# Kernel optimization log

Measured on AMD Instinct MI355X. Metric: run time of the kernel, lower is better.

Reference implementation:

```python
import jax, jax.numpy as jnp
import numpy as np

B, T, D = 4, 1024, 1024   # batch, block_size, d_model
H, HS = 16, 64            # n_head, head_size


def setup_inputs() -> dict:
    key = jax.random.key(0)
    ks = jax.random.split(key, 6)
    s = 0.02  # small init like nn.Linear default scale
    return {
        "x": jax.random.normal(ks[0], (B, T, D), jnp.float32),
        "Wq": jax.random.normal(ks[1], (H, D, HS), jnp.float32) * s,
        "Wk": jax.random.normal(ks[2], (H, D, HS), jnp.float32) * s,
        "Wv": jax.random.normal(ks[3], (H, D, HS), jnp.float32) * s,
        "Wo": jax.random.normal(ks[4], (H * HS, D), jnp.float32) * s,
        "bo": jnp.zeros((D,), jnp.float32),
    }


def reference(x, Wq, Wk, Wv, Wo, bo):
    # Batched equivalent of the per-head loop: all heads in one einsum.
    q = jnp.einsum('btd,hde->bhte', x, Wq)   # [B,H,T,HS]
    k = jnp.einsum('btd,hde->bhte', x, Wk)
    v = jnp.einsum('btd,hde->bhte', x, Wv)
    scores = jnp.einsum('bhte,bhse->bhts', q, k) * (HS ** -0.5)  # [B,H,T,T]
    causal = jnp.tril(jnp.ones((T, T), dtype=bool))
    scores = jnp.where(causal, scores, -jnp.inf)
    att = jax.nn.softmax(scores, axis=-1)
    out = jnp.einsum('bhts,bhse->bhte', att, v)                  # [B,H,T,HS]
    out = out.transpose(0, 2, 1, 3).reshape(B, T, H * HS)        # concat heads
    return out @ Wo + bo                                         # proj to d_model
```

## Files before the change

kernel.cpp:

```cpp
#include <hip/hip_runtime.h>
#include <math.h>

#define NB 4
#define SEQ 1024
#define DM 1024
#define NH 16
#define HS 64

typedef __attribute__((ext_vector_type(8))) short short8;
typedef __attribute__((ext_vector_type(4))) short short4v;
typedef __attribute__((ext_vector_type(4))) float floatx4;

#define MFMA(a, b, c) __builtin_amdgcn_mfma_f32_16x16x32_bf16((a), (b), (c), 0, 0, 0)

static __device__ __forceinline__ unsigned short f2bf(float f) {
  unsigned int u = __float_as_uint(f);
  u += 0x7FFFu + ((u >> 16) & 1u);
  return (unsigned short)(u >> 16);
}
static __device__ __forceinline__ unsigned short f2bf_fast(float f) {
  return (unsigned short)((__float_as_uint(f) + 0x8000u) >> 16);
}

static __device__ __forceinline__ void g2l(const unsigned short* g, short* l) {
  __builtin_amdgcn_global_load_lds(
      (const __attribute__((address_space(1))) void*)g,
      (__attribute__((address_space(3))) void*)l, 16, 0, 0);
}

#define SWZ_SRC(tid) ((((tid) & 7) ^ (((tid) >> 3) & 7)) << 3)
#define SWZ_RD(B, r) ((((B) ^ ((r) & 7)) << 3))

__global__ __launch_bounds__(256) void prep_all(
    const float* __restrict__ x,
    const float* __restrict__ Wq, const float* __restrict__ Wk,
    const float* __restrict__ Wv, const float* __restrict__ Wo,
    unsigned short* __restrict__ xb,
    unsigned short* __restrict__ Wtq, unsigned short* __restrict__ Wtk,
    unsigned short* __restrict__ Wtv, unsigned short* __restrict__ Wot) {
  __shared__ __align__(16) short Ts[64 * 72];
  const int tid = threadIdx.x;
  const int mat = blockIdx.y;
  if (mat == 4) {
    int base = blockIdx.x * 4096;
#pragma unroll
    for (int i = 0; i < 16; i++) {
      int idx4 = base + tid + i * 256;
      float4 v = *(const float4*)(x + (size_t)idx4 * 4);
      short4v o;
      o[0] = (short)f2bf(v.x); o[1] = (short)f2bf(v.y);
      o[2] = (short)f2bf(v.z); o[3] = (short)f2bf(v.w);
      *(short4v*)(xb + (size_t)idx4 * 4) = o;
    }
    return;
  }
  const float* src;
  unsigned short* dst;
  int r0, c0;
  if (mat < 3) {
    src = (mat == 0) ? Wq : (mat == 1) ? Wk : Wv;
    dst = (mat == 0) ? Wtq : (mat == 1) ? Wtk : Wtv;
    int h = blockIdx.x >> 4;
    int d0 = (blockIdx.x & 15) * 64;
    src += (size_t)(h * DM + d0) * HS;
    dst += (size_t)(h * HS) * DM + d0;
    r0 = HS;  c0 = DM;
  } else {
    src = Wo; dst = Wot;
    int k0 = (blockIdx.x >> 4) * 64;
    int n0 = (blockIdx.x & 15) * 64;
    src += (size_t)k0 * DM + n0;
    dst += (size_t)n0 * DM + k0;
    r0 = DM;  c0 = DM;
  }
#pragma unroll
  for (int i = 0; i < 4; i++) {
    int p = tid + i * 256;
    int row = p >> 4, c4 = (p & 15) << 2;
    float4 v = *(const float4*)(src + (size_t)row * r0 + c4);
    Ts[(c4 + 0) * 72 + row] = (short)f2bf(v.x);
    Ts[(c4 + 1) * 72 + row] = (short)f2bf(v.y);
    Ts[(c4 + 2) * 72 + row] = (short)f2bf(v.z);
    Ts[(c4 + 3) * 72 + row] = (short)f2bf(v.w);
  }
  __syncthreads();
#pragma unroll
  for (int i = 0; i < 2; i++) {
    int p = tid + i * 256;
    int row = p >> 3, c8 = (p & 7) << 3;
    *(short8*)(dst + (size_t)row * c0 + c8) = *(const short8*)&Ts[row * 72 + c8];
  }
}

__global__ __launch_bounds__(256, 3) void qkv_gemm128(
    const unsigned short* __restrict__ xb,
    const unsigned short* __restrict__ Wcat,
    unsigned short* __restrict__ qo,
    unsigned short* __restrict__ ko,
    unsigned short* __restrict__ vo) {
  __shared__ __align__(16) short As[128 * 64];
  __shared__ __align__(16) short Bs[128 * 64];
  const int tid = threadIdx.x;
  const int bm = blockIdx.x, bn = blockIdx.y;
  const int lane = tid & 63, wave = tid >> 6;
  const int quad = lane >> 4, l16 = lane & 15;
  const int wr = wave >> 1, wc = wave & 1;
  const int l7 = l16 & 7;
  const floatx4 fzero = {0.f, 0.f, 0.f, 0.f};

  floatx4 acc[4][4];
#pragma unroll
  for (int i = 0; i < 4; i++)
#pragma unroll
    for (int j = 0; j < 4; j++) acc[i][j] = fzero;

  const int srow = tid >> 3;
  const int scolw = SWZ_SRC(tid);
  const unsigned short* Ag = xb + (size_t)(bm * 128 + srow) * DM + scolw;
  const unsigned short* Bg = Wcat + (size_t)(bn * 128 + srow) * DM + scolw;
  short* Ad = As + tid * 8;
  short* Bd = Bs + tid * 8;

  for (int k0 = 0; k0 < DM; k0 += 64) {
    __syncthreads();
#pragma unroll
    for (int i = 0; i < 4; i++) g2l(Ag + (size_t)i * 32 * DM + k0, Ad + i * 2048);
#pragma unroll
    for (int i = 0; i < 4; i++) g2l(Bg + (size_t)i * 32 * DM + k0, Bd + i * 2048);
    __syncthreads();

    short8 af[4][2], bf[4][2];
#pragma unroll
    for (int ti = 0; ti < 4; ti++)
#pragma unroll
      for (int kh = 0; kh < 2; kh++)
        af[ti][kh] = *(const short8*)&As[(wr * 64 + ti * 16 + l16) * 64 +
                                          SWZ_RD(kh * 4 + quad, l7)];
#pragma unroll
    for (int tj = 0; tj < 4; tj++)
#pragma unroll
      for (int kh = 0; kh < 2; kh++)
        bf[tj][kh] = *(const short8*)&Bs[(wc * 64 + tj * 16 + l16) * 64 +
                                          SWZ_RD(kh * 4 + quad, l7)];
#pragma unroll
    for (int ti = 0; ti < 4; ti++)
#pragma unroll
      for (int tj = 0; tj < 4; tj++) {
        acc[ti][tj] = MFMA(af[ti][0], bf[tj][0], acc[ti][tj]);
        acc[ti][tj] = MFMA(af[ti][1], bf[tj][1], acc[ti][tj]);
      }
  }

  const int mat = bn >> 3;
  const int mbase = bm * 128 + wr * 64 + quad * 4;
  const int nn0 = (bn & 7) * 128 + wc * 64;
  if (mat < 2) {
    unsigned short* dst = (mat == 0) ? qo : ko;
#pragma unroll
    for (int ti = 0; ti < 4; ti++)
#pragma unroll
      for (int tj = 0; tj < 4; tj++) {
        int ecol = nn0 + tj * 16 + l16;
        int h = ecol >> 6, e = ecol & 63;
#pragma unroll
        for (int r = 0; r < 4; r++) {
          int m = mbase + ti * 16 + r;
          int b = m >> 10, t = m & (SEQ - 1);
          dst[((size_t)(b * NH + h) * SEQ + t) * HS + e] = f2bf_fast(acc[ti][tj][r]);
        }
      }
  } else {
#pragma unroll
    for (int ti = 0; ti < 4; ti++)
#pragma unroll
      for (int tj = 0; tj < 4; tj++) {
        int ecol = nn0 + tj * 16 + l16;
        int h = ecol >> 6, e = ecol & 63;
        int m0 = mbase + ti * 16;
        int b = m0 >> 10, t0 = m0 & (SEQ - 1);
        short4v pv;
#pragma unroll
        for (int r = 0; r < 4; r++) pv[r] = (short)f2bf_fast(acc[ti][tj][r]);
        *(short4v*)&vo[((size_t)(b * NH + h) * HS + e) * SEQ + t0] = pv;
      }
  }
}

__global__ __launch_bounds__(256) void attn_kernel(
    const unsigned short* __restrict__ q,
    const unsigned short* __restrict__ k,
    const unsigned short* __restrict__ v,
    unsigned short* __restrict__ o)
{
  __shared__ __align__(16) short Ks[64 * 64];
  __shared__ __align__(16) short Vt[64 * 64];
  __shared__ __align__(16) short Ps[64 * 76];
  const int tid = threadIdx.x;
  const int lid = (int)blockIdx.x;
  const int g = lid >> 8, cc = lid & 255;
  const int j = cc >> 6, bhid = cc & 63;
  const int qt = (g == 0) ? j : (g == 1) ? 15 - j : (g == 2) ? 7 - j : 8 + j;
  const int h = bhid & 15, b = bhid >> 4;
  const int lane = tid & 63, wave = tid >> 6;
  const int quad = lane >> 4, l16 = lane & 15;
  const int l7 = l16 & 7;
  const size_t bh = (size_t)(b * NH + h) * SEQ * HS;
  const unsigned short* qp = q + bh + (size_t)qt * 64 * HS;
  const unsigned short* kbase = k + bh;
  const unsigned short* vbase = v + (size_t)(b * NH + h) * HS * SEQ;
  const floatx4 fzero = {0.f, 0.f, 0.f, 0.f};
  const float c2 = 0.125f * 1.44269504089f;
  const float C0 = 16.0f * 1.44269504089f;
  const int srow = tid >> 3;
  const int scolw = SWZ_SRC(tid);

  short8 qa[2];
  qa[0] = *(const short8*)(qp + (size_t)(wave * 16 + l16) * HS + quad * 8);
  qa[1] = *(const short8*)(qp + (size_t)(wave * 16 + l16) * HS + 32 + quad * 8);

#pragma unroll
  for (int i = 0; i < 2; i++) {
    g2l(kbase + (size_t)(srow + i * 32) * HS + scolw, Ks + tid * 8 + i * 2048);
    g2l(vbase + (size_t)(srow + i * 32) * SEQ + scolw, Vt + tid * 8 + i * 2048);
  }
  __syncthreads();

  const int rowbase = qt * 64 + wave * 16;
  float l_[4];
  floatx4 O[4];
#pragma unroll
  for (int r = 0; r < 4; r++) l_[r] = 0.f;
#pragma unroll
  for (int tj = 0; tj < 4; tj++) O[tj] = fzero;

  for (int kt = 0; kt <= qt; kt++) {
    floatx4 S[4];
#pragma unroll
    for (int tj = 0; tj < 4; tj++) {
      short8 b0 = *(const short8*)&Ks[(tj * 16 + l16) * 64 + SWZ_RD(quad, l7)];
      short8 b1 = *(const short8*)&Ks[(tj * 16 + l16) * 64 + SWZ_RD(4 + quad, l7)];
      floatx4 s = fzero;
      s = MFMA(qa[0], b0, s);
      s = MFMA(qa[1], b1, s);
      S[tj] = s;
    }
    if (kt == qt) {
#pragma unroll
      for (int tj = 0; tj < 4; tj++) {
        int col = kt * 64 + tj * 16 + l16;
#pragma unroll
        for (int r = 0; r < 4; r++) {
          int row = rowbase + quad * 4 + r;
          if (col > row) S[tj][r] = -INFINITY;
        }
      }
    }
#pragma unroll
    for (int tj = 0; tj < 4; tj++)
#pragma unroll
      for (int r = 0; r < 4; r++) {
        float pv = __builtin_amdgcn_exp2f(S[tj][r] * c2 - C0);
        l_[r] += pv;
        Ps[(wave * 16 + quad * 4 + r) * 76 + tj * 16 + l16] =
            (short)(unsigned short)((__float_as_uint(pv) + 0x8000u) >> 16);
      }

    short8 pa[2];
#pragma unroll
    for (int kh = 0; kh < 2; kh++)
      pa[kh] = *(const short8*)&Ps[(wave * 16 + l16) * 76 + kh * 32 + quad * 8];
#pragma unroll
    for (int tj = 0; tj < 4; tj++) {
      short8 b0 = *(const short8*)&Vt[(tj * 16 + l16) * 64 + SWZ_RD(quad, l7)];
      short8 b1 = *(const short8*)&Vt[(tj * 16 + l16) * 64 + SWZ_RD(4 + quad, l7)];
      O[tj] = MFMA(pa[0], b0, O[tj]);
      O[tj] = MFMA(pa[1], b1, O[tj]);
    }

    if (kt < qt) {
      __syncthreads();
#pragma unroll
      for (int i = 0; i < 2; i++) {
        g2l(kbase + (size_t)(kt + 1) * 64 * HS + (size_t)(srow + i * 32) * HS + scolw,
            Ks + tid * 8 + i * 2048);
        g2l(vbase + (size_t)(srow + i * 32) * SEQ + (kt + 1) * 64 + scolw,
            Vt + tid * 8 + i * 2048);
      }
      __syncthreads();
    }
  }

#pragma unroll
  for (int r = 0; r < 4; r++) {
    float lsum = l_[r];
#pragma unroll
    for (int off = 1; off < 16; off <<= 1)
      lsum += __shfl_xor(lsum, off, 16);
    float inv = 1.0f / lsum;
#pragma unroll
    for (int tj = 0; tj < 4; tj++)
      Ps[(wave * 16 + quad * 4 + r) * 76 + tj * 16 + l16] =
          (short)f2bf_fast(O[tj][r] * inv);
  }
  __syncthreads();
  {
    const int row = tid >> 2;
    const int c16 = (tid & 3) * 16;
    unsigned short* dst = o + ((size_t)(b * SEQ + qt * 64 + row)) * DM + h * HS + c16;
    const short* src = &Ps[row * 76 + c16];
#pragma unroll
    for (int u = 0; u < 4; u++)
      *(short4v*)(dst + u * 4) = *(const short4v*)(src + u * 4);
  }
}

__global__ __launch_bounds__(256, 3) void out_gemm64(
    const unsigned short* __restrict__ A,
    const unsigned short* __restrict__ Bt,
    const float* __restrict__ bo,
    float* __restrict__ out) {
  __shared__ __align__(16) short As[128 * 64];
  __shared__ __align__(16) short Bs[64 * 64];
  const int tid = threadIdx.x;
  const int bm = blockIdx.x, bn = blockIdx.y;
  const int lane = tid & 63, wave = tid >> 6;
  const int quad = lane >> 4, l16 = lane & 15;
  const int wr = wave >> 1, wc = wave & 1;
  const int l7 = l16 & 7;
  const floatx4 fzero = {0.f, 0.f, 0.f, 0.f};

  floatx4 acc[4][2];
#pragma unroll
  for (int i = 0; i < 4; i++)
#pragma unroll
    for (int j = 0; j < 2; j++) acc[i][j] = fzero;

  const int srow = tid >> 3;
  const int scolw = SWZ_SRC(tid);
  const unsigned short* Ag = A + (size_t)(bm * 128 + srow) * DM + scolw;
  const unsigned short* Bg = Bt + (size_t)(bn * 64 + srow) * DM + scolw;
  short* Ad = As + tid * 8;
  short* Bd = Bs + tid * 8;

  for (int k0 = 0; k0 < DM; k0 += 64) {
    __syncthreads();
#pragma unroll
    for (int i = 0; i < 4; i++) g2l(Ag + (size_t)i * 32 * DM + k0, Ad + i * 2048);
#pragma unroll
    for (int i = 0; i < 2; i++) g2l(Bg + (size_t)i * 32 * DM + k0, Bd + i * 2048);
    __syncthreads();

    short8 af[4][2], bf[2][2];
#pragma unroll
    for (int ti = 0; ti < 4; ti++)
#pragma unroll
      for (int kh = 0; kh < 2; kh++)
        af[ti][kh] = *(const short8*)&As[(wr * 64 + ti * 16 + l16) * 64 +
                                          SWZ_RD(kh * 4 + quad, l7)];
#pragma unroll
    for (int tj = 0; tj < 2; tj++)
#pragma unroll
      for (int kh = 0; kh < 2; kh++)
        bf[tj][kh] = *(const short8*)&Bs[(wc * 32 + tj * 16 + l16) * 64 +
                                          SWZ_RD(kh * 4 + quad, l7)];
#pragma unroll
    for (int ti = 0; ti < 4; ti++)
#pragma unroll
      for (int tj = 0; tj < 2; tj++) {
        acc[ti][tj] = MFMA(af[ti][0], bf[tj][0], acc[ti][tj]);
        acc[ti][tj] = MFMA(af[ti][1], bf[tj][1], acc[ti][tj]);
      }
  }

#pragma unroll
  for (int ti = 0; ti < 4; ti++)
#pragma unroll
    for (int tj = 0; tj < 2; tj++) {
      int n = bn * 64 + wc * 32 + tj * 16 + l16;
      float bias = bo[n];
#pragma unroll
      for (int r = 0; r < 4; r++) {
        int m = bm * 128 + wr * 64 + ti * 16 + quad * 4 + r;
        out[(size_t)m * DM + n] = acc[ti][tj][r] + bias;
      }
    }
}

extern "C" void kernel_launch(void* const* d_in, const int* in_sizes, int n_in,
                              void* d_out, int out_size, void* d_ws, size_t ws_size,
                              hipStream_t stream) {
  const float* x  = (const float*)d_in[0];
  const float* Wq = (const float*)d_in[1];
  const float* Wk = (const float*)d_in[2];
  const float* Wv = (const float*)d_in[3];
  const float* Wo = (const float*)d_in[4];
  const float* bo = (const float*)d_in[5];
  float* out = (float*)d_out;

  const size_t nx = (size_t)NB * SEQ * DM;
  const size_t nw = (size_t)DM * DM;
  unsigned short* xb  = (unsigned short*)d_ws;
  unsigned short* wtq = xb + nx;
  unsigned short* wtk = wtq + nw;
  unsigned short* wtv = wtk + nw;
  unsigned short* wot = wtv + nw;
  unsigned short* qws = wot + nw;
  unsigned short* kws = qws + nx;
  unsigned short* vws = kws + nx;
  unsigned short* aws = vws + nx;

  prep_all<<<dim3(256, 5), dim3(256), 0, stream>>>(x, Wq, Wk, Wv, Wo,
                                                   xb, wtq, wtk, wtv, wot);
  qkv_gemm128<<<dim3(32, 24), dim3(256), 0, stream>>>(xb, wtq, qws, kws, vws);
  attn_kernel<<<dim3(1024), dim3(256), 0, stream>>>(qws, kws, vws, aws);
  out_gemm64<<<dim3(32, 16), dim3(256), 0, stream>>>(aws, wot, bo, out);
}
```

Measured before the change: 151.9 us.

## Load K/V fragments directly from global into registers, two waves of 32 rows

The attention kernel no longer stages K and V tiles in shared memory. Each lane now loads its MFMA fragments straight from global memory (relying on cache), which removes the two block-wide barriers per key tile. The block shrinks to two waves, each covering 32 query rows, so every loaded K/V fragment is reused across two 16-row sub-tiles. In exchange the kernel issues redundant global loads per wave, has no prefetch of the next tile, and needs more registers for the doubled accumulators.

```diff
diff --git a/kernel.cpp b/kernel.cpp
--- a/kernel.cpp
+++ b/kernel.cpp
@@ -186,14 +186,12 @@
   }
 }
 
-__global__ __launch_bounds__(256) void attn_kernel(
+__global__ __launch_bounds__(128) void attn_kernel(
     const unsigned short* __restrict__ q,
     const unsigned short* __restrict__ k,
     const unsigned short* __restrict__ v,
     unsigned short* __restrict__ o)
 {
-  __shared__ __align__(16) short Ks[64 * 64];
-  __shared__ __align__(16) short Vt[64 * 64];
   __shared__ __align__(16) short Ps[64 * 76];
   const int tid = threadIdx.x;
   const int lid = (int)blockIdx.x;
@@ -203,7 +201,6 @@
   const int h = bhid & 15, b = bhid >> 4;
   const int lane = tid & 63, wave = tid >> 6;
   const int quad = lane >> 4, l16 = lane & 15;
-  const int l7 = l16 & 7;
   const size_t bh = (size_t)(b * NH + h) * SEQ * HS;
   const unsigned short* qp = q + bh + (size_t)qt * 64 * HS;
   const unsigned short* kbase = k + bh;
@@ -211,105 +208,99 @@
   const floatx4 fzero = {0.f, 0.f, 0.f, 0.f};
   const float c2 = 0.125f * 1.44269504089f;
   const float C0 = 16.0f * 1.44269504089f;
-  const int srow = tid >> 3;
-  const int scolw = SWZ_SRC(tid);
-
-  short8 qa[2];
-  qa[0] = *(const short8*)(qp + (size_t)(wave * 16 + l16) * HS + quad * 8);
-  qa[1] = *(const short8*)(qp + (size_t)(wave * 16 + l16) * HS + 32 + quad * 8);
-
-#pragma unroll
-  for (int i = 0; i < 2; i++) {
-    g2l(kbase + (size_t)(srow + i * 32) * HS + scolw, Ks + tid * 8 + i * 2048);
-    g2l(vbase + (size_t)(srow + i * 32) * SEQ + scolw, Vt + tid * 8 + i * 2048);
-  }
-  __syncthreads();
-
-  const int rowbase = qt * 64 + wave * 16;
-  float l_[4];
-  floatx4 O[4];
-#pragma unroll
-  for (int r = 0; r < 4; r++) l_[r] = 0.f;
-#pragma unroll
-  for (int tj = 0; tj < 4; tj++) O[tj] = fzero;
+
+  short8 qa[2][2];
+#pragma unroll
+  for (int ih = 0; ih < 2; ih++)
+#pragma unroll
+    for (int kh = 0; kh < 2; kh++)
+      qa[ih][kh] = *(const short8*)(qp + (size_t)(wave * 32 + ih * 16 + l16) * HS +
+                                    kh * 32 + quad * 8);
+
+  const int rowbase = qt * 64 + wave * 32;
+  float l_[2][4];
+  floatx4 O[2][4];
+#pragma unroll
+  for (int ih = 0; ih < 2; ih++)
+#pragma unroll
+    for (int r = 0; r < 4; r++) l_[ih][r] = 0.f;
+#pragma unroll
+  for (int ih = 0; ih < 2; ih++)
+#pragma unroll
+    for (int tj = 0; tj < 4; tj++) O[ih][tj] = fzero;
 
   for (int kt = 0; kt <= qt; kt++) {
-    floatx4 S[4];
-#pragma unroll
-    for (int tj = 0; tj < 4; tj++) {
-      short8 b0 = *(const short8*)&Ks[(tj * 16 + l16) * 64 + SWZ_RD(quad, l7)];
-      short8 b1 = *(const short8*)&Ks[(tj * 16 + l16) * 64 + SWZ_RD(4 + quad, l7)];
-      floatx4 s = fzero;
-      s = MFMA(qa[0], b0, s);
-      s = MFMA(qa[1], b1, s);
-      S[tj] = s;
+    const unsigned short* kp = kbase + (size_t)kt * 64 * HS;
+    const unsigned short* vp = vbase + kt * 64;
+    short8 kb[4][2], vb[4][2];
+#pragma unroll
+    for (int tj = 0; tj < 4; tj++)
+#pragma unroll
+      for (int kh = 0; kh < 2; kh++) {
+        kb[tj][kh] = *(const short8*)(kp + (size_t)(tj * 16 + l16) * HS +
+                                      kh * 32 + quad * 8);
+        vb[tj][kh] = *(const short8*)(vp + (size_t)(tj * 16 + l16) * SEQ +
+                                      kh * 32 + quad * 8);
+      }
+    const bool diag = (kt == qt);
+#pragma unroll
+    for (int ih = 0; ih < 2; ih++)
+#pragma unroll
+      for (int tj = 0; tj < 4; tj++) {
+        floatx4 s = MFMA(qa[ih][0], kb[tj][0], fzero);
+        s = MFMA(qa[ih][1], kb[tj][1], s);
+        if (diag) {
+          int col = tj * 16 + l16;
+#pragma unroll
+          for (int r = 0; r < 4; r++)
+            if (col > wave * 32 + ih * 16 + quad * 4 + r) s[r] = -INFINITY;
+        }
+#pragma unroll
+        for (int r = 0; r < 4; r++) {
+          float pv = __builtin_amdgcn_exp2f(s[r] * c2 - C0);
+          l_[ih][r] += pv;
+          Ps[(wave * 32 + ih * 16 + quad * 4 + r) * 76 + tj * 16 + l16] =
+              (short)(unsigned short)((__float_as_uint(pv) + 0x8000u) >> 16);
+        }
+      }
+    short8 pa[2][2];
+#pragma unroll
+    for (int ih = 0; ih < 2; ih++)
+#pragma unroll
+      for (int kh = 0; kh < 2; kh++)
+        pa[ih][kh] = *(const short8*)&Ps[(wave * 32 + ih * 16 + l16) * 76 +
+                                          kh * 32 + quad * 8];
+#pragma unroll
+    for (int tj = 0; tj < 4; tj++)
+#pragma unroll
+      for (int ih = 0; ih < 2; ih++) {
+        O[ih][tj] = MFMA(pa[ih][0], vb[tj][0], O[ih][tj]);
+        O[ih][tj] = MFMA(pa[ih][1], vb[tj][1], O[ih][tj]);
+      }
+  }
+
+#pragma unroll
+  for (int ih = 0; ih < 2; ih++)
+#pragma unroll
+    for (int r = 0; r < 4; r++) {
+      float lsum = l_[ih][r];
+#pragma unroll
+      for (int off = 1; off < 16; off <<= 1)
+        lsum += __shfl_xor(lsum, off, 16);
+      float inv = 1.0f / lsum;
+#pragma unroll
+      for (int tj = 0; tj < 4; tj++)
+        Ps[(wave * 32 + ih * 16 + quad * 4 + r) * 76 + tj * 16 + l16] =
+            (short)f2bf_fast(O[ih][tj][r] * inv);
     }
-    if (kt == qt) {
-#pragma unroll
-      for (int tj = 0; tj < 4; tj++) {
-        int col = kt * 64 + tj * 16 + l16;
-#pragma unroll
-        for (int r = 0; r < 4; r++) {
-          int row = rowbase + quad * 4 + r;
-          if (col > row) S[tj][r] = -INFINITY;
-        }
-      }
-    }
-#pragma unroll
-    for (int tj = 0; tj < 4; tj++)
-#pragma unroll
-      for (int r = 0; r < 4; r++) {
-        float pv = __builtin_amdgcn_exp2f(S[tj][r] * c2 - C0);
-        l_[r] += pv;
-        Ps[(wave * 16 + quad * 4 + r) * 76 + tj * 16 + l16] =
-            (short)(unsigned short)((__float_as_uint(pv) + 0x8000u) >> 16);
-      }
-
-    short8 pa[2];
-#pragma unroll
-    for (int kh = 0; kh < 2; kh++)
-      pa[kh] = *(const short8*)&Ps[(wave * 16 + l16) * 76 + kh * 32 + quad * 8];
-#pragma unroll
-    for (int tj = 0; tj < 4; tj++) {
-      short8 b0 = *(const short8*)&Vt[(tj * 16 + l16) * 64 + SWZ_RD(quad, l7)];
-      short8 b1 = *(const short8*)&Vt[(tj * 16 + l16) * 64 + SWZ_RD(4 + quad, l7)];
-      O[tj] = MFMA(pa[0], b0, O[tj]);
-      O[tj] = MFMA(pa[1], b1, O[tj]);
-    }
-
-    if (kt < qt) {
-      __syncthreads();
-#pragma unroll
-      for (int i = 0; i < 2; i++) {
-        g2l(kbase + (size_t)(kt + 1) * 64 * HS + (size_t)(srow + i * 32) * HS + scolw,
-            Ks + tid * 8 + i * 2048);
-        g2l(vbase + (size_t)(srow + i * 32) * SEQ + (kt + 1) * 64 + scolw,
-            Vt + tid * 8 + i * 2048);
-      }
-      __syncthreads();
-    }
-  }
-
-#pragma unroll
-  for (int r = 0; r < 4; r++) {
-    float lsum = l_[r];
-#pragma unroll
-    for (int off = 1; off < 16; off <<= 1)
-      lsum += __shfl_xor(lsum, off, 16);
-    float inv = 1.0f / lsum;
-#pragma unroll
-    for (int tj = 0; tj < 4; tj++)
-      Ps[(wave * 16 + quad * 4 + r) * 76 + tj * 16 + l16] =
-          (short)f2bf_fast(O[tj][r] * inv);
-  }
   __syncthreads();
   {
-    const int row = tid >> 2;
-    const int c16 = (tid & 3) * 16;
-    unsigned short* dst = o + ((size_t)(b * SEQ + qt * 64 + row)) * DM + h * HS + c16;
-    const short* src = &Ps[row * 76 + c16];
-#pragma unroll
-    for (int u = 0; u < 4; u++)
+    const int row = tid >> 1;
+    const int c32 = (tid & 1) * 32;
+    unsigned short* dst = o + ((size_t)(b * SEQ + qt * 64 + row)) * DM + h * HS + c32;
+    const short* src = &Ps[row * 76 + c32];
+#pragma unroll
+    for (int u = 0; u < 8; u++)
       *(short4v*)(dst + u * 4) = *(const short4v*)(src + u * 4);
   }
 }
@@ -412,6 +403,6 @@
   prep_all<<<dim3(256, 5), dim3(256), 0, stream>>>(x, Wq, Wk, Wv, Wo,
                                                    xb, wtq, wtk, wtv, wot);
   qkv_gemm128<<<dim3(32, 24), dim3(256), 0, stream>>>(xb, wtq, qws, kws, vws);
-  attn_kernel<<<dim3(1024), dim3(256), 0, stream>>>(qws, kws, vws, aws);
+  attn_kernel<<<dim3(1024), dim3(128), 0, stream>>>(qws, kws, vws, aws);
   out_gemm64<<<dim3(32, 16), dim3(256), 0, stream>>>(aws, wot, bo, out);
 }
```

Measured after the change: 168.4 us. 10.9% more time.
